# Performance work log

Measured on AMD Instinct MI355X. Metric: run time of the kernel, lower is better.

## Reference

```python
import jax, jax.numpy as jnp
import numpy as np

SIGMA = 0.5   # pairwise density bandwidth (density_std)
EPS = 1e-8
B, N, K, P, D, F, H = 8, 20, 2, 320, 3, 64, 64


def setup_inputs() -> dict:
    key = jax.random.key(0)
    ks = jax.random.split(key, 8)
    # ring graph: neighbor node index for each of the K=2 incident slots
    nbr = np.stack([(np.arange(N) - 1) % N, (np.arange(N) + 1) % N], axis=1).astype(np.int32)
    return {
        "X": jax.random.uniform(ks[0], (B, N, K, P, D), minval=-1.0, maxval=1.0),
        "W": jax.random.uniform(ks[1], (B, N, K, P), minval=0.1, maxval=1.0),
        "feats": jax.random.normal(ks[2], (B, N, F)),
        "mu": 0.1 * jax.random.normal(ks[3], (N, K, D)),
        "W1": jax.random.normal(ks[4], (N, F, H)) / np.sqrt(F),
        "Wx": jax.random.normal(ks[5], (N, D, H)) / np.sqrt(D),
        "b1": jnp.zeros((N, H), jnp.float32),
        "W2": jax.random.normal(ks[6], (N, H)) / np.sqrt(H),
        "bias2": jnp.zeros((N,), jnp.float32),
        "nbr_idx": jnp.asarray(nbr),
    }


def reference(X, W, feats, mu, W1, Wx, b1, W2, bias2, nbr_idx):
    # X: [B,N,K,P,D] belief/message particles, W: [B,N,K,P] particle weights
    Bs, Ns, Ks, Ps, Ds = X.shape
    KP = Ks * Ps
    # normalize incoming message weights per node (as in uniform_init: sum over K*P == 1)
    Wn = W / (W.sum(axis=(2, 3), keepdims=True) + EPS)
    Xf = X.reshape(Bs, Ns, KP, Ds)
    Wf = Wn.reshape(Bs, Ns, KP)
    # irregular gather of each node's neighbors' particles/weights
    Xn = Xf[:, nbr_idx]   # [B,N,K,KP,D]
    Wnb = Wf[:, nbr_idx]  # [B,N,K,KP]
    # pairwise edge density: Gaussian on (x_dst - mu_e) vs x_src, via ||a||^2+||b||^2-2ab
    a = X - mu[None, :, :, None, :]                      # [B,N,K,P,D]
    cross = jnp.einsum('bnkpd,bnkqd->bnkpq', a, Xn)      # [B,N,K,P,KP]
    d2 = (a * a).sum(-1)[..., None] + (Xn * Xn).sum(-1)[..., None, :] - 2.0 * cross
    kern = jnp.exp(-d2 / (2.0 * SIGMA * SIGMA))
    # neighbor message: weighted density sum over neighbor particles
    msg = jnp.einsum('bnkpq,bnkq->bnkp', kern, Wnb)      # [B,N,K,P]
    # per-node unary likelihood MLP on (image features, particle state)
    hf = jnp.einsum('bnf,nfh->bnh', feats, W1)           # [B,N,H]
    hx = jnp.einsum('bnkpd,ndh->bnkph', X, Wx)           # [B,N,K,P,H]
    h = jax.nn.relu(hf[:, :, None, None, :] + hx + b1[None, :, None, None, :])
    u = jax.nn.sigmoid(jnp.einsum('bnkph,nh->bnkp', h, W2) + bias2[None, :, None, None])
    # belief weight update: unary * neighbor message, renormalized per node
    w = u * msg
    return w / (w.sum(axis=(2, 3), keepdims=True) + EPS)
```

## Files before the change

### kernel.cpp

```cpp
#include <hip/hip_runtime.h>
#include <hip/hip_bf16.h>

constexpr int B_ = 8, N_ = 20, K_ = 2, P_ = 320, D_ = 3, F_ = 64, H_ = 64;
constexpr int Q_ = K_ * P_;
constexpr float EPS_ = 1e-8f;
constexpr float LOG2E_ = 1.4426950408889634f;

typedef float v2f __attribute__((ext_vector_type(2)));

__device__ __forceinline__ v2f mk2(float a, float b) { v2f r; r.x = a; r.y = b; return r; }

__device__ __forceinline__ v2f pk_fma(v2f a, v2f b, v2f c) {
    v2f d;
    asm("v_pk_fma_f32 %0, %1, %2, %3" : "=v"(d) : "v"(a), "v"(b), "v"(c));
    return d;
}

__global__ __launch_bounds__(Q_) void dnbp_kernel(
    const float* __restrict__ X,
    const float* __restrict__ W,
    const float* __restrict__ feats,
    const float* __restrict__ mu,
    const float* __restrict__ W1,
    const float* __restrict__ Wx,
    const float* __restrict__ b1,
    const float* __restrict__ W2,
    const float* __restrict__ bias2,
    const int* __restrict__ nbr,
    float* __restrict__ out)
{
    __shared__ float4 xnA[K_][Q_ / 2];
    __shared__ float4 xnB[K_][Q_ / 2];
    __shared__ float4 gA[H_ / 2];
    __shared__ float4 gB[H_ / 2];
    __shared__ v2f    hb2[H_ / 2];
    __shared__ float  red[2 * 10];
    __shared__ float  sumW[2];
    __shared__ float  totalS;

    const int bn  = blockIdx.x;
    const int b   = bn / N_;
    const int n   = bn - b * N_;
    const int tid = threadIdx.x;
    const int wave = tid >> 6;
    const int lane = tid & 63;

    const int j0 = nbr[n * 2 + 0];
    const int j1 = nbr[n * 2 + 1];

    if (tid < H_) {
        const int h = tid;
        const float* fp  = feats + ((size_t)b * N_ + n) * F_;
        const float* w1p = W1 + (size_t)n * F_ * H_ + h;
        float acc = 0.f;
        #pragma unroll 8
        for (int f = 0; f < F_; ++f)
            acc = fmaf(fp[f], w1p[(size_t)f * H_], acc);
        const int hi = h >> 1, ho = h & 1;
        ((float*)&hb2[hi])[ho] = acc + b1[n * H_ + h];
        const float* wxp = Wx + (size_t)n * D_ * H_ + h;
        float* ga = (float*)&gA[hi];
        float* gb = (float*)&gB[hi];
        ga[ho]     = wxp[0];
        ga[2 + ho] = wxp[H_];
        gb[ho]     = wxp[2 * H_];
        gb[2 + ho] = W2[n * H_ + h];
    }

    const int q  = tid;
    const int qi = q >> 1, qo = q & 1;
    float w0, w1, ew0, ew1;
    {
        const size_t base0 = ((size_t)b * N_ + j0) * Q_ + q;
        const float* xp = X + base0 * D_;
        const float x0 = xp[0], x1 = xp[1], x2 = xp[2];
        const float sq = x0 * x0 + x1 * x1 + x2 * x2;
        w0  = W[base0];
        ew0 = __builtin_amdgcn_exp2f(-2.f * LOG2E_ * sq);
        float* a  = (float*)&xnA[0][qi];
        float* bq = (float*)&xnB[0][qi];
        a[qo] = x0; a[2 + qo] = x1; bq[qo] = x2;
    }
    {
        const size_t base1 = ((size_t)b * N_ + j1) * Q_ + q;
        const float* xp = X + base1 * D_;
        const float x0 = xp[0], x1 = xp[1], x2 = xp[2];
        const float sq = x0 * x0 + x1 * x1 + x2 * x2;
        w1  = W[base1];
        ew1 = __builtin_amdgcn_exp2f(-2.f * LOG2E_ * sq);
        float* a  = (float*)&xnA[1][qi];
        float* bq = (float*)&xnB[1][qi];
        a[qo] = x0; a[2 + qo] = x1; bq[qo] = x2;
    }

    {
        float v0 = w0, v1 = w1;
        #pragma unroll
        for (int off = 32; off > 0; off >>= 1) {
            v0 += __shfl_down(v0, off, 64);
            v1 += __shfl_down(v1, off, 64);
        }
        if (lane == 0) { red[wave * 2] = v0; red[wave * 2 + 1] = v1; }
        __syncthreads();
        if (tid == 0) {
            float s0 = 0.f, s1 = 0.f;
            #pragma unroll
            for (int wv = 0; wv < 10; ++wv) { s0 += red[wv * 2]; s1 += red[wv * 2 + 1]; }
            sumW[0] = 1.f / (s0 + EPS_);
            sumW[1] = 1.f / (s1 + EPS_);
        }
        __syncthreads();
    }

    ((float*)&xnB[0][qi])[2 + qo] = w0 * ew0 * sumW[0];
    ((float*)&xnB[1][qi])[2 + qo] = w1 * ew1 * sumW[1];
    __syncthreads();

    const int k = (tid >= P_) ? 1 : 0;
    const int p = tid - k * P_;
    const size_t rowbase = (((size_t)b * N_ + n) * K_ + k) * P_ + p;
    const float* xp = X + rowbase * D_;
    const float x0 = xp[0], x1 = xp[1], x2 = xp[2];
    const float* mup = mu + (n * K_ + k) * D_;
    const float a0 = x0 - mup[0];
    const float a1 = x1 - mup[1];
    const float a2 = x2 - mup[2];
    const float ra2 = a0 * a0 + a1 * a1 + a2 * a2;
    const v2f S0 = mk2(a0 * (4.f * LOG2E_), a0 * (4.f * LOG2E_));
    const v2f S1 = mk2(a1 * (4.f * LOG2E_), a1 * (4.f * LOG2E_));
    const v2f S2 = mk2(a2 * (4.f * LOG2E_), a2 * (4.f * LOG2E_));
    const v2f RA = mk2(-2.f * LOG2E_ * ra2, -2.f * LOG2E_ * ra2);

    const v2f X0v = mk2(x0, x0), X1v = mk2(x1, x1), X2v = mk2(x2, x2);
    v2f acc2 = mk2(0.f, 0.f);
    #pragma unroll 4
    for (int i = 0; i < H_ / 2; ++i) {
        const float4 ga = gA[i];
        const float4 gb = gB[i];
        const v2f   hb = hb2[i];
        v2f t = pk_fma(X0v, mk2(ga.x, ga.y),
                pk_fma(X1v, mk2(ga.z, ga.w),
                pk_fma(X2v, mk2(gb.x, gb.y), hb)));
        t.x = fmaxf(t.x, 0.f);
        t.y = fmaxf(t.y, 0.f);
        acc2 = pk_fma(t, mk2(gb.z, gb.w), acc2);
    }
    const float logit = bias2[n] + acc2.x + acc2.y;
    const float u = 1.f / (1.f + __expf(-logit));

    const float4* __restrict__ pA = xnA[k];
    const float4* __restrict__ pB = xnB[k];
    v2f m0 = mk2(0.f, 0.f), m1 = mk2(0.f, 0.f);
    #pragma unroll 2
    for (int t2 = 0; t2 < Q_ / 2; t2 += 2) {
        const float4 A0 = pA[t2], A1 = pA[t2 + 1];
        const float4 B0 = pB[t2], B1 = pB[t2 + 1];
        v2f d0 = pk_fma(mk2(A0.x, A0.y), S0,
                 pk_fma(mk2(A0.z, A0.w), S1,
                 pk_fma(mk2(B0.x, B0.y), S2, RA)));
        v2f d1 = pk_fma(mk2(A1.x, A1.y), S0,
                 pk_fma(mk2(A1.z, A1.w), S1,
                 pk_fma(mk2(B1.x, B1.y), S2, RA)));
        v2f e0 = mk2(__builtin_amdgcn_exp2f(d0.x), __builtin_amdgcn_exp2f(d0.y));
        v2f e1 = mk2(__builtin_amdgcn_exp2f(d1.x), __builtin_amdgcn_exp2f(d1.y));
        m0 = pk_fma(mk2(B0.z, B0.w), e0, m0);
        m1 = pk_fma(mk2(B1.z, B1.w), e1, m1);
    }
    const float msg = (m0.x + m0.y) + (m1.x + m1.y);
    const float wval = u * msg;

    {
        float v = wval;
        #pragma unroll
        for (int off = 32; off > 0; off >>= 1) v += __shfl_down(v, off, 64);
        if (lane == 0) red[wave] = v;
        __syncthreads();
        if (tid == 0) {
            float s = 0.f;
            #pragma unroll
            for (int wv = 0; wv < 10; ++wv) s += red[wv];
            totalS = 1.f / (s + EPS_);
        }
        __syncthreads();
    }

    out[((size_t)b * N_ + n) * Q_ + tid] = wval * totalS;
}

extern "C" void kernel_launch(void* const* d_in, const int* in_sizes, int n_in,
                              void* d_out, int out_size, void* d_ws, size_t ws_size,
                              hipStream_t stream) {
    const float* X     = (const float*)d_in[0];
    const float* W     = (const float*)d_in[1];
    const float* feats = (const float*)d_in[2];
    const float* mu    = (const float*)d_in[3];
    const float* W1    = (const float*)d_in[4];
    const float* Wx    = (const float*)d_in[5];
    const float* b1    = (const float*)d_in[6];
    const float* W2    = (const float*)d_in[7];
    const float* bias2 = (const float*)d_in[8];
    const int*   nbr   = (const int*)d_in[9];
    float*       out   = (float*)d_out;

    dnbp_kernel<<<B_ * N_, Q_, 0, stream>>>(X, W, feats, mu, W1, Wx, b1, W2,
                                            bias2, nbr, out);
}
```

Measured before the change: 96.50 us.

## Register-block pairwise density loop over four rows per thread with LDS partial sums

```diff
diff --git a/kernel.cpp b/kernel.cpp
--- a/kernel.cpp
+++ b/kernel.cpp
@@ -29,8 +29,10 @@
     const int* __restrict__ nbr,
     float* __restrict__ out)
 {
-    __shared__ float4 xnA[K_][Q_ / 2];
-    __shared__ float4 xnB[K_][Q_ / 2];
+    __shared__ float4 xnA[K_][P_];
+    __shared__ float4 xnB[K_][P_];
+    __shared__ float4 aTab[Q_];
+    __shared__ float  part[Q_][4];
     __shared__ float4 gA[H_ / 2];
     __shared__ float4 gB[H_ / 2];
     __shared__ v2f    hb2[H_ / 2];
@@ -93,6 +95,22 @@
         a[qo] = x0; a[2 + qo] = x1; bq[qo] = x2;
     }
 
+    const int kk = (tid >= P_) ? 1 : 0;
+    const int pp = tid - kk * P_;
+    float x0o, x1o, x2o;
+    {
+        const size_t rowbase = (((size_t)b * N_ + n) * K_ + kk) * P_ + pp;
+        const float* xp = X + rowbase * D_;
+        x0o = xp[0]; x1o = xp[1]; x2o = xp[2];
+        const float* mup = mu + (n * K_ + kk) * D_;
+        const float a0 = x0o - mup[0];
+        const float a1 = x1o - mup[1];
+        const float a2 = x2o - mup[2];
+        const float ra2 = a0 * a0 + a1 * a1 + a2 * a2;
+        aTab[tid] = make_float4(a0 * (4.f * LOG2E_), a1 * (4.f * LOG2E_),
+                                a2 * (4.f * LOG2E_), -2.f * LOG2E_ * ra2);
+    }
+
     {
         float v0 = w0, v1 = w1;
         #pragma unroll
@@ -116,22 +134,49 @@
     ((float*)&xnB[1][qi])[2 + qo] = w1 * ew1 * sumW[1];
     __syncthreads();
 
-    const int k = (tid >= P_) ? 1 : 0;
-    const int p = tid - k * P_;
-    const size_t rowbase = (((size_t)b * N_ + n) * K_ + k) * P_ + p;
-    const float* xp = X + rowbase * D_;
-    const float x0 = xp[0], x1 = xp[1], x2 = xp[2];
-    const float* mup = mu + (n * K_ + k) * D_;
-    const float a0 = x0 - mup[0];
-    const float a1 = x1 - mup[1];
-    const float a2 = x2 - mup[2];
-    const float ra2 = a0 * a0 + a1 * a1 + a2 * a2;
-    const v2f S0 = mk2(a0 * (4.f * LOG2E_), a0 * (4.f * LOG2E_));
-    const v2f S1 = mk2(a1 * (4.f * LOG2E_), a1 * (4.f * LOG2E_));
-    const v2f S2 = mk2(a2 * (4.f * LOG2E_), a2 * (4.f * LOG2E_));
-    const v2f RA = mk2(-2.f * LOG2E_ * ra2, -2.f * LOG2E_ * ra2);
-
-    const v2f X0v = mk2(x0, x0), X1v = mk2(x1, x1), X2v = mk2(x2, x2);
+    const int base = tid & ~3;
+    const int qt   = tid & 3;
+    const float4* __restrict__ tabA = xnA[kk];
+    const float4* __restrict__ tabB = xnB[kk];
+
+    v2f S0[4], S1[4], S2[4], RA[4];
+    #pragma unroll
+    for (int j = 0; j < 4; ++j) {
+        const float4 av = aTab[base + j];
+        S0[j] = mk2(av.x, av.x);
+        S1[j] = mk2(av.y, av.y);
+        S2[j] = mk2(av.z, av.z);
+        RA[j] = mk2(av.w, av.w);
+    }
+    v2f acc[4];
+    #pragma unroll
+    for (int j = 0; j < 4; ++j) acc[j] = mk2(0.f, 0.f);
+
+    #pragma unroll 2
+    for (int i = 0; i < P_ / 4; ++i) {
+        const int pi = 4 * i + qt;
+        const float4 A  = tabA[pi];
+        const float4 Bv = tabB[pi];
+        #pragma unroll
+        for (int j = 0; j < 4; ++j) {
+            const v2f d = pk_fma(mk2(A.x, A.y), S0[j],
+                          pk_fma(mk2(A.z, A.w), S1[j],
+                          pk_fma(mk2(Bv.x, Bv.y), S2[j], RA[j])));
+            const v2f e = mk2(__builtin_amdgcn_exp2f(d.x),
+                              __builtin_amdgcn_exp2f(d.y));
+            acc[j] = pk_fma(mk2(Bv.z, Bv.w), e, acc[j]);
+        }
+    }
+    #pragma unroll
+    for (int j = 0; j < 4; ++j)
+        part[base + j][qt] = acc[j].x + acc[j].y;
+
+    __syncthreads();
+
+    const float* pr = part[tid];
+    const float msg = (pr[0] + pr[1]) + (pr[2] + pr[3]);
+
+    const v2f X0v = mk2(x0o, x0o), X1v = mk2(x1o, x1o), X2v = mk2(x2o, x2o);
     v2f acc2 = mk2(0.f, 0.f);
     #pragma unroll 4
     for (int i = 0; i < H_ / 2; ++i) {
@@ -147,26 +192,6 @@
     }
     const float logit = bias2[n] + acc2.x + acc2.y;
     const float u = 1.f / (1.f + __expf(-logit));
-
-    const float4* __restrict__ pA = xnA[k];
-    const float4* __restrict__ pB = xnB[k];
-    v2f m0 = mk2(0.f, 0.f), m1 = mk2(0.f, 0.f);
-    #pragma unroll 2
-    for (int t2 = 0; t2 < Q_ / 2; t2 += 2) {
-        const float4 A0 = pA[t2], A1 = pA[t2 + 1];
-        const float4 B0 = pB[t2], B1 = pB[t2 + 1];
-        v2f d0 = pk_fma(mk2(A0.x, A0.y), S0,
-                 pk_fma(mk2(A0.z, A0.w), S1,
-                 pk_fma(mk2(B0.x, B0.y), S2, RA)));
-        v2f d1 = pk_fma(mk2(A1.x, A1.y), S0,
-                 pk_fma(mk2(A1.z, A1.w), S1,
-                 pk_fma(mk2(B1.x, B1.y), S2, RA)));
-        v2f e0 = mk2(__builtin_amdgcn_exp2f(d0.x), __builtin_amdgcn_exp2f(d0.y));
-        v2f e1 = mk2(__builtin_amdgcn_exp2f(d1.x), __builtin_amdgcn_exp2f(d1.y));
-        m0 = pk_fma(mk2(B0.z, B0.w), e0, m0);
-        m1 = pk_fma(mk2(B1.z, B1.w), e1, m1);
-    }
-    const float msg = (m0.x + m0.y) + (m1.x + m1.y);
     const float wval = u * msg;
 
     {
```

Result: faster. 93.73 us (-2.9%).
